# Optimization experiments

Hardware: AMD Instinct MI355X
Metric: run time of the kernel (lower is better)

The kernel has to match this reference:

```python
import jax, jax.numpy as jnp
import numpy as np

B, L, D = 8, 2048, 256
NEG = 10000.0


def setup_inputs() -> dict:
    key = jax.random.key(0)
    kq, kk, kv, km = jax.random.split(key, 4)
    return {
        "query": jax.random.normal(kq, (B, L, D), dtype=jnp.float32),
        "key": jax.random.normal(kk, (B, L, D), dtype=jnp.float32),
        "value": jax.random.normal(kv, (B, L, D), dtype=jnp.float32),
        "mask": jax.random.randint(km, (B, L), 0, 2).astype(bool),
    }


def reference(query, key, value, mask):
    d = query.shape[-1]
    # scores: [B, Lq, Lk]
    e = jnp.einsum("bqd,bkd->bqk", query, key) / jnp.sqrt(jnp.asarray(d, query.dtype))
    # history_only (causal) mask: subtract 10000 where key index > query index
    q_len, k_len = query.shape[1], key.shape[1]
    causal = (jnp.arange(k_len)[None, :] > jnp.arange(q_len)[:, None]).astype(query.dtype)
    e = e - NEG * causal[None, :, :]
    # key padding mask: [B, 1, Lk]
    e = e - NEG * (1.0 - mask.astype(query.dtype))[:, None, :]
    attn = jax.nn.softmax(e, axis=-1)
    return jnp.einsum("bqk,bkd->bqd", attn, value)
```

## Files before the change

kernel.cpp:

```cpp
#include <hip/hip_runtime.h>
#include <stdint.h>

#define NL 2048
#define ND 256
#define KVB 32
#define QB 64
#define NQT 32
#define NT_ALL (NL / KVB)
#define CHUNK 10
#define NCHUNKS_B 125
#define TILE_BYTES (KVB * ND * 2)
#define IMG (8 * NT_ALL * TILE_BYTES)
#define WS_MB 256
#define WS_K (WS_MB + 2048)
#define WS_V (WS_K + IMG)
#define WS_P (WS_V + IMG)
#define PART_BYTES (QB * ND * 2 + QB * 8)

typedef __attribute__((ext_vector_type(8))) short short8;
typedef __attribute__((ext_vector_type(4))) short short4v;
typedef __attribute__((ext_vector_type(4))) float f32x4;
typedef __attribute__((ext_vector_type(4))) unsigned int u32x4;
typedef __attribute__((ext_vector_type(8))) unsigned short ushort8;

__device__ __forceinline__ unsigned short bf16rne(float x) {
  unsigned u = __builtin_bit_cast(unsigned, x);
  u += 0x7FFFu + ((u >> 16) & 1u);
  return (unsigned short)(u >> 16);
}

__device__ __forceinline__ short8 cvt8(float4 a, float4 b, float scale) {
  short8 v;
  v[0] = (short)bf16rne(a.x * scale);
  v[1] = (short)bf16rne(a.y * scale);
  v[2] = (short)bf16rne(a.z * scale);
  v[3] = (short)bf16rne(a.w * scale);
  v[4] = (short)bf16rne(b.x * scale);
  v[5] = (short)bf16rne(b.y * scale);
  v[6] = (short)bf16rne(b.z * scale);
  v[7] = (short)bf16rne(b.w * scale);
  return v;
}

__global__ __launch_bounds__(512)
void mask_pack(const unsigned* __restrict__ M, unsigned* __restrict__ MB) {
  __shared__ int badS;
  if (threadIdx.x == 0) badS = 0;
  __syncthreads();
  bool bad = false;
  for (int i = threadIdx.x; i < 4096; i += 512)
    if (M[i] > 1u) bad = true;
  if (__any(bad) && (threadIdx.x & 63) == 0) badS = 1;
  __syncthreads();
  const int byteMode = badS;
  const int i = threadIdx.x;
  unsigned m = 0;
  for (int j = 0; j < 32; ++j) {
    int mv = byteMode ? (int)((const unsigned char*)M)[i * 32 + j] : (int)M[i * 32 + j];
    m |= (mv ? 1u : 0u) << j;
  }
  MB[i] = m;
}

__global__ __launch_bounds__(128)
void convert_kv(const float* __restrict__ K, const float* __restrict__ V,
                unsigned char* __restrict__ ws) {
  const int t = blockIdx.x;
  const int b = t >> 6, tix = t & 63;
  const float* kt = K + ((size_t)b * NL + tix * KVB) * ND;
  const float* vt = V + ((size_t)b * NL + tix * KVB) * ND;
  unsigned char* kd = ws + WS_K + (size_t)t * TILE_BYTES;
  unsigned char* vd = ws + WS_V + (size_t)t * TILE_BYTES;
#pragma unroll
  for (int it = 0; it < 8; ++it) {
    int idx = it * 128 + threadIdx.x;
    int row = idx >> 5, u = idx & 31, f = u * 8;
    const float4* kp = (const float4*)(kt + (size_t)row * ND + f);
    int kb = (row * 512 + f * 2) ^ ((row & 7) << 4);
    *(short8*)(kd + kb) = cvt8(kp[0], kp[1], 1.0f);
    const float4* vp = (const float4*)(vt + (size_t)row * ND + f);
    int vb = (row >> 2) * 2048 + (u >> 1) * 128 + (row & 3) * 32 + (u & 1) * 16;
    *(short8*)(vd + vb) = cvt8(vp[0], vp[1], 1.0f);
  }
}

__global__ __launch_bounds__(256, 2)
void attn_fwd(const float* __restrict__ Qg, const unsigned* __restrict__ MBg,
              unsigned char* ws) {
  __shared__ unsigned short Ks[2][KVB * ND];
  __shared__ unsigned short Vs[2][KVB * ND];

  const int tid = threadIdx.x;
  const int wv = tid >> 6;
  const int lane = tid & 63;
  const int g = lane >> 4;
  const int cc = lane & 15;

  const int fid = blockIdx.x;
  const int b = fid / NCHUNKS_B;
  int rem = fid - b * NCHUNKS_B;
  int qt = 0, c = 0, pbase = 0;
  if (rem < 7) {
    qt = 0; c = rem; pbase = 0;
  } else {
    rem -= 7; pbase = 7;
    for (qt = 1; qt < NQT; ++qt) {
      int ncq = (2 * qt + 2 + CHUNK - 1) / CHUNK;
      if (rem < ncq) { c = rem; break; }
      rem -= ncq; pbase += ncq;
    }
  }
  const int qb = qt * QB;
  const int nt_s = (qt == 0) ? NT_ALL : (2 * qt + 2);
  const int t0 = c * CHUNK;
  const int t1 = min(nt_s, t0 + CHUNK);
  unsigned char* pp = ws + WS_P + (size_t)(b * NCHUNKS_B + pbase + c) * PART_BYTES;
  unsigned short* ppA = (unsigned short*)pp;
  float* ppM = (float*)(pp + QB * ND * 2);
  float* ppL = ppM + QB;

  auto stage_tile = [&](int tix, int bi) {
    const unsigned char* kg = ws + WS_K + ((size_t)(b * NT_ALL + tix)) * TILE_BYTES;
    const unsigned char* vg = ws + WS_V + ((size_t)(b * NT_ALL + tix)) * TILE_BYTES;
#pragma unroll
    for (int s = 0; s < 4; ++s) {
      const int seg = wv * 4 + s;
      __builtin_amdgcn_global_load_lds(
          (const __attribute__((address_space(1))) unsigned int*)(kg + seg * 1024 + lane * 16),
          (__attribute__((address_space(3))) unsigned int*)((unsigned char*)&Ks[bi][0] + seg * 1024),
          16, 0, 0);
      __builtin_amdgcn_global_load_lds(
          (const __attribute__((address_space(1))) unsigned int*)(vg + seg * 1024 + lane * 16),
          (__attribute__((address_space(3))) unsigned int*)((unsigned char*)&Vs[bi][0] + seg * 1024),
          16, 0, 0);
    }
  };

  const float* qp = Qg + ((size_t)b * NL + (qb + 16 * wv + cc)) * ND;
  short8 qf[8];
#pragma unroll
  for (int ch = 0; ch < 8; ++ch) {
    int f = ch * 32 + g * 8;
    float4 a0 = *reinterpret_cast<const float4*>(qp + f);
    float4 a1 = *reinterpret_cast<const float4*>(qp + f + 4);
    qf[ch] = cvt8(a0, a1, 0.0625f);
  }
  const int qg = qb + 16 * wv + cc;

  f32x4 acc[16];
#pragma unroll
  for (int i = 0; i < 16; ++i) acc[i] = (f32x4){0.f, 0.f, 0.f, 0.f};
  float m_run = -3.0e38f, l_run = 0.f;

  int buf = 0;
  stage_tile(t0, 0);
  __syncthreads();

  for (int tix = t0; tix < t1; ++tix) {
    if (tix + 1 < t1) stage_tile(tix + 1, buf ^ 1);
    const int kv0 = tix * KVB;
    const unsigned mb = MBg[b * NT_ALL + tix];

    const char* ksB = (const char*)&Ks[buf][0];
    f32x4 s0 = {0.f, 0.f, 0.f, 0.f}, s1 = {0.f, 0.f, 0.f, 0.f};
    __builtin_amdgcn_s_setprio(1);
#pragma unroll
    for (int ch = 0; ch < 8; ++ch) {
      int cbase = ch * 64 + g * 16;
      int b0 = (cc * 512 + cbase) ^ ((cc & 7) << 4);
      int b1 = ((cc + 16) * 512 + cbase) ^ ((cc & 7) << 4);
      short8 k0 = *reinterpret_cast<const short8*>(ksB + b0);
      short8 k1 = *reinterpret_cast<const short8*>(ksB + b1);
      s0 = __builtin_amdgcn_mfma_f32_16x16x32_bf16(k0, qf[ch], s0, 0, 0, 0);
      s1 = __builtin_amdgcn_mfma_f32_16x16x32_bf16(k1, qf[ch], s1, 0, 0, 0);
    }
    __builtin_amdgcn_s_setprio(0);

#pragma unroll
    for (int r = 0; r < 4; ++r) {
      int k0i = 4 * g + r, k1i = 16 + 4 * g + r;
      if (!((mb >> k0i) & 1u)) s0[r] -= 10000.f;
      if (!((mb >> k1i) & 1u)) s1[r] -= 10000.f;
      if (kv0 + k0i > qg) s0[r] -= 10000.f;
      if (kv0 + k1i > qg) s1[r] -= 10000.f;
    }

    float rmax = fmaxf(fmaxf(fmaxf(s0[0], s0[1]), fmaxf(s0[2], s0[3])),
                       fmaxf(fmaxf(s1[0], s1[1]), fmaxf(s1[2], s1[3])));
    rmax = fmaxf(rmax, __shfl_xor(rmax, 16));
    rmax = fmaxf(rmax, __shfl_xor(rmax, 32));
    bool grow = (rmax > m_run + 8.f);
    if (__any(grow)) {
      float mn = fmaxf(m_run, rmax);
      float alpha = __expf(m_run - mn);
      m_run = mn;
      l_run *= alpha;
      f32x4 av;
#pragma unroll
      for (int r = 0; r < 4; ++r) av[r] = __shfl(alpha, 20 * g + r);
#pragma unroll
      for (int i = 0; i < 16; ++i) acc[i] *= av;
    }
    float p0[4], p1[4];
#pragma unroll
    for (int r = 0; r < 4; ++r) {
      p0[r] = __expf(s0[r] - m_run);
      p1[r] = __expf(s1[r] - m_run);
    }
    float rsum = (p0[0] + p0[1]) + (p0[2] + p0[3]) +
                 (p1[0] + p1[1]) + (p1[2] + p1[3]);
    rsum += __shfl_xor(rsum, 16);
    rsum += __shfl_xor(rsum, 32);
    l_run += rsum;

    unsigned a0, a1, b0w, b1w;
    asm("v_cvt_pk_bf16_f32 %0, %1, %2" : "=v"(a0) : "v"(p0[0]), "v"(p0[1]));
    asm("v_cvt_pk_bf16_f32 %0, %1, %2" : "=v"(a1) : "v"(p0[2]), "v"(p0[3]));
    asm("v_cvt_pk_bf16_f32 %0, %1, %2" : "=v"(b0w) : "v"(p1[0]), "v"(p1[1]));
    asm("v_cvt_pk_bf16_f32 %0, %1, %2" : "=v"(b1w) : "v"(p1[2]), "v"(p1[3]));
    const int srcLo = cc + ((g & 1) << 5);
    const int srcHi = srcLo + 16;
    unsigned wa0 = (unsigned)__shfl((int)a0, srcLo);
    unsigned wa1 = (unsigned)__shfl((int)a1, srcLo);
    unsigned wa2 = (unsigned)__shfl((int)a0, srcHi);
    unsigned wa3 = (unsigned)__shfl((int)a1, srcHi);
    unsigned wb0 = (unsigned)__shfl((int)b0w, srcLo);
    unsigned wb1 = (unsigned)__shfl((int)b1w, srcLo);
    unsigned wb2 = (unsigned)__shfl((int)b0w, srcHi);
    unsigned wb3 = (unsigned)__shfl((int)b1w, srcHi);
    const bool hiHalf = (g >= 2);
    u32x4 paw = {hiHalf ? wb0 : wa0, hiHalf ? wb1 : wa1,
                 hiHalf ? wb2 : wa2, hiHalf ? wb3 : wa3};
    short8 pa = __builtin_bit_cast(short8, paw);

    const unsigned va = (unsigned)(uintptr_t)&Vs[buf][0] + g * 4096 + cc * 8;
    short4v lo[16], hi[16];
#pragma unroll
    for (int ft = 0; ft < 16; ++ft) {
      asm volatile("ds_read_b64_tr_b16 %0, %1 offset:%2"
                   : "=&v"(lo[ft]) : "v"(va), "i"(ft * 128) : "memory");
      asm volatile("ds_read_b64_tr_b16 %0, %1 offset:%2"
                   : "=&v"(hi[ft]) : "v"(va), "i"(ft * 128 + 2048) : "memory");
    }
    asm volatile("s_waitcnt lgkmcnt(15)" ::: "memory");
    __builtin_amdgcn_sched_barrier(0);
    __builtin_amdgcn_s_setprio(1);
#pragma unroll
    for (int ft = 0; ft < 8; ++ft) {
      short8 vb = __builtin_shufflevector(lo[ft], hi[ft], 0, 1, 2, 3, 4, 5, 6, 7);
      acc[ft] = __builtin_amdgcn_mfma_f32_16x16x32_bf16(pa, vb, acc[ft], 0, 0, 0);
    }
    __builtin_amdgcn_s_setprio(0);
    asm volatile("s_waitcnt lgkmcnt(0)" ::: "memory");
    __builtin_amdgcn_sched_barrier(0);
    __builtin_amdgcn_s_setprio(1);
#pragma unroll
    for (int ft = 8; ft < 16; ++ft) {
      short8 vb = __builtin_shufflevector(lo[ft], hi[ft], 0, 1, 2, 3, 4, 5, 6, 7);
      acc[ft] = __builtin_amdgcn_mfma_f32_16x16x32_bf16(pa, vb, acc[ft], 0, 0, 0);
    }
    __builtin_amdgcn_s_setprio(0);

    __syncthreads();
    buf ^= 1;
  }

  unsigned short* sc = &Ks[0][0];
#pragma unroll
  for (int ft = 0; ft < 16; ++ft) {
#pragma unroll
    for (int r = 0; r < 4; ++r) {
      sc[(16 * wv + 4 * g + r) * 256 + ft * 16 + cc] = bf16rne(acc[ft][r]);
    }
  }
  if (g == 0) {
    ppM[16 * wv + cc] = m_run;
    ppL[16 * wv + cc] = l_run;
  }
  __syncthreads();
  {
    const int row = tid >> 2, q4 = tid & 3;
    const unsigned short* srow = sc + row * 256 + q4 * 64;
#pragma unroll
    for (int kk = 0; kk < 8; ++kk) {
      *(ushort8*)(ppA + (size_t)row * ND + q4 * 64 + kk * 8) =
          *(const ushort8*)(srow + kk * 8);
    }
  }
}

__global__ __launch_bounds__(256)
void attn_combine(const unsigned char* __restrict__ ws, float* __restrict__ Og) {
  const int bid = blockIdx.x;
  const int b = bid >> 5, qt = bid & 31;
  const int tid = threadIdx.x;
  const int row = tid >> 2, sub = tid & 3;

  int pbase = 0, nc = 7;
  if (qt > 0) {
    pbase = 7;
    for (int j = 1; j < qt; ++j) pbase += (2 * j + 2 + CHUNK - 1) / CHUNK;
    nc = (2 * qt + 2 + CHUNK - 1) / CHUNK;
  }
  const unsigned char* p0 = ws + WS_P + (size_t)(b * NCHUNKS_B + pbase) * PART_BYTES;

  float M = -3.0e38f;
  for (int c = 0; c < nc; ++c) {
    M = fmaxf(M, *(const float*)(p0 + (size_t)c * PART_BYTES + QB * ND * 2 + row * 4));
  }
  float L = 0.f;
  float o[64];
#pragma unroll
  for (int j = 0; j < 64; ++j) o[j] = 0.f;
  for (int c = 0; c < nc; ++c) {
    const unsigned char* pc = p0 + (size_t)c * PART_BYTES;
    float mm = *(const float*)(pc + QB * ND * 2 + row * 4);
    float ll = *(const float*)(pc + QB * ND * 2 + QB * 4 + row * 4);
    float s = __expf(mm - M);
    L += ll * s;
    const unsigned short* pa =
        (const unsigned short*)pc + (size_t)row * ND + sub * 64;
#pragma unroll
    for (int kk = 0; kk < 8; ++kk) {
      ushort8 a = *(const ushort8*)(pa + kk * 8);
#pragma unroll
      for (int j = 0; j < 8; ++j) {
        unsigned u = ((unsigned)a[j]) << 16;
        o[kk * 8 + j] += __builtin_bit_cast(float, u) * s;
      }
    }
  }
  const float invL = 1.0f / L;
  float* op = Og + ((size_t)b * NL + qt * QB + row) * ND + sub * 64;
#pragma unroll
  for (int kk = 0; kk < 16; ++kk) {
    float4 v = {o[kk * 4] * invL, o[kk * 4 + 1] * invL, o[kk * 4 + 2] * invL,
                o[kk * 4 + 3] * invL};
    *(float4*)(op + kk * 4) = v;
  }
}

extern "C" void kernel_launch(void* const* d_in, const int* in_sizes, int n_in,
                              void* d_out, int out_size, void* d_ws, size_t ws_size,
                              hipStream_t stream) {
  (void)in_sizes; (void)n_in; (void)out_size; (void)ws_size;
  const float* Q = (const float*)d_in[0];
  const float* K = (const float*)d_in[1];
  const float* V = (const float*)d_in[2];
  const int* M = (const int*)d_in[3];
  unsigned char* ws = (unsigned char*)d_ws;

  mask_pack<<<dim3(1), dim3(512), 0, stream>>>((const unsigned*)M,
                                               (unsigned*)(ws + WS_MB));
  convert_kv<<<dim3(512), dim3(128), 0, stream>>>(K, V, ws);
  attn_fwd<<<dim3(8 * NCHUNKS_B), dim3(256), 0, stream>>>(
      Q, (const unsigned*)(ws + WS_MB), ws);
  attn_combine<<<dim3(256), dim3(256), 0, stream>>>(ws, (float*)d_out);
}
```

Baseline: 103.1 us.

## Triple-buffer K tiles with explicit vmcnt waits and defer row-sum reduction

Splits K and V staging so K tiles are prefetched two iterations ahead in a triple buffer while V stays double-buffered. __syncthreads is replaced with explicit s_waitcnt vmcnt counts plus raw s_barrier, so only the needed loads are waited on. The per-iteration cross-lane row-sum shuffles are also moved out of the loop and done once at the end. This costs an extra 16KB of LDS per block, which may reduce occupancy from the intended two blocks per CU, and it relies on exact vmcnt counting for correctness.

New measurement: 102.1 us. Within noise of the previous version (-1.0%).

```diff
diff --git a/kernel.cpp b/kernel.cpp
--- a/kernel.cpp
+++ b/kernel.cpp
@@ -87,7 +87,7 @@
 __global__ __launch_bounds__(256, 2)
 void attn_fwd(const float* __restrict__ Qg, const unsigned* __restrict__ MBg,
               unsigned char* ws) {
-  __shared__ unsigned short Ks[2][KVB * ND];
+  __shared__ unsigned short Ks[3][KVB * ND];
   __shared__ unsigned short Vs[2][KVB * ND];
 
   const int tid = threadIdx.x;
@@ -119,9 +119,8 @@
   float* ppM = (float*)(pp + QB * ND * 2);
   float* ppL = ppM + QB;
 
-  auto stage_tile = [&](int tix, int bi) {
+  auto stage_K = [&](int tix, int bi) {
     const unsigned char* kg = ws + WS_K + ((size_t)(b * NT_ALL + tix)) * TILE_BYTES;
-    const unsigned char* vg = ws + WS_V + ((size_t)(b * NT_ALL + tix)) * TILE_BYTES;
 #pragma unroll
     for (int s = 0; s < 4; ++s) {
       const int seg = wv * 4 + s;
@@ -129,6 +128,13 @@
           (const __attribute__((address_space(1))) unsigned int*)(kg + seg * 1024 + lane * 16),
           (__attribute__((address_space(3))) unsigned int*)((unsigned char*)&Ks[bi][0] + seg * 1024),
           16, 0, 0);
+    }
+  };
+  auto stage_V = [&](int tix, int bi) {
+    const unsigned char* vg = ws + WS_V + ((size_t)(b * NT_ALL + tix)) * TILE_BYTES;
+#pragma unroll
+    for (int s = 0; s < 4; ++s) {
+      const int seg = wv * 4 + s;
       __builtin_amdgcn_global_load_lds(
           (const __attribute__((address_space(1))) unsigned int*)(vg + seg * 1024 + lane * 16),
           (__attribute__((address_space(3))) unsigned int*)((unsigned char*)&Vs[bi][0] + seg * 1024),
@@ -152,16 +158,30 @@
   for (int i = 0; i < 16; ++i) acc[i] = (f32x4){0.f, 0.f, 0.f, 0.f};
   float m_run = -3.0e38f, l_run = 0.f;
 
-  int buf = 0;
-  stage_tile(t0, 0);
-  __syncthreads();
+  asm volatile("s_waitcnt vmcnt(0)" ::: "memory");
+  __builtin_amdgcn_sched_barrier(0);
+  stage_K(t0, t0 % 3);
+  if (t0 + 1 < t1) stage_K(t0 + 1, (t0 + 1) % 3);
+  stage_V(t0, t0 & 1);
 
   for (int tix = t0; tix < t1; ++tix) {
-    if (tix + 1 < t1) stage_tile(tix + 1, buf ^ 1);
+    if (tix + 2 < t1) stage_K(tix + 2, (tix + 2) % 3);
+    if (tix + 1 < t1) stage_V(tix + 1, (tix + 1) & 1);
+    if (tix + 2 < t1) {
+      asm volatile("s_waitcnt vmcnt(8)" ::: "memory");
+    } else if (tix + 1 < t1) {
+      asm volatile("s_waitcnt vmcnt(4)" ::: "memory");
+    } else {
+      asm volatile("s_waitcnt vmcnt(0)" ::: "memory");
+    }
+    __builtin_amdgcn_sched_barrier(0);
+    __builtin_amdgcn_s_barrier();
+    __builtin_amdgcn_sched_barrier(0);
+
     const int kv0 = tix * KVB;
     const unsigned mb = MBg[b * NT_ALL + tix];
 
-    const char* ksB = (const char*)&Ks[buf][0];
+    const char* ksB = (const char*)&Ks[tix % 3][0];
     f32x4 s0 = {0.f, 0.f, 0.f, 0.f}, s1 = {0.f, 0.f, 0.f, 0.f};
     __builtin_amdgcn_s_setprio(1);
 #pragma unroll
@@ -207,11 +227,8 @@
       p0[r] = __expf(s0[r] - m_run);
       p1[r] = __expf(s1[r] - m_run);
     }
-    float rsum = (p0[0] + p0[1]) + (p0[2] + p0[3]) +
-                 (p1[0] + p1[1]) + (p1[2] + p1[3]);
-    rsum += __shfl_xor(rsum, 16);
-    rsum += __shfl_xor(rsum, 32);
-    l_run += rsum;
+    l_run += (p0[0] + p0[1]) + (p0[2] + p0[3]) +
+             (p1[0] + p1[1]) + (p1[2] + p1[3]);
 
     unsigned a0, a1, b0w, b1w;
     asm("v_cvt_pk_bf16_f32 %0, %1, %2" : "=v"(a0) : "v"(p0[0]), "v"(p0[1]));
@@ -233,7 +250,7 @@
                  hiHalf ? wb2 : wa2, hiHalf ? wb3 : wa3};
     short8 pa = __builtin_bit_cast(short8, paw);
 
-    const unsigned va = (unsigned)(uintptr_t)&Vs[buf][0] + g * 4096 + cc * 8;
+    const unsigned va = (unsigned)(uintptr_t)&Vs[tix & 1][0] + g * 4096 + cc * 8;
     short4v lo[16], hi[16];
 #pragma unroll
     for (int ft = 0; ft < 16; ++ft) {
@@ -261,9 +278,13 @@
     }
     __builtin_amdgcn_s_setprio(0);
 
-    __syncthreads();
-    buf ^= 1;
-  }
+    __builtin_amdgcn_sched_barrier(0);
+    __builtin_amdgcn_s_barrier();
+    __builtin_amdgcn_sched_barrier(0);
+  }
+
+  l_run += __shfl_xor(l_run, 16);
+  l_run += __shfl_xor(l_run, 32);
 
   unsigned short* sc = &Ks[0][0];
 #pragma unroll
```
